# Performance work log

Measured on AMD Instinct MI355X. Metric: run time of the kernel, lower is better.

## Reference

```python
import jax, jax.numpy as jnp
import numpy as np

IMG = 128
NEAR, FAR = 1.0, 100.0
BG_EPS = 1e-3      # eps in soft_rasterize: background depth logit
SIGMA = 1e-6       # sigma_val
DIST_EPS = 1e-4    # dist_eps
GAMMA = 1e-6       # gamma_val
CHUNK = 500
B, V, F = 1, 5023, 10000


def setup_inputs():
    key = jax.random.key(0)
    k1, k2, k3, k4 = jax.random.split(key, 4)
    xy = jax.random.uniform(k1, (B, V, 2), minval=-1.0, maxval=1.0, dtype=jnp.float32)
    z = jax.random.uniform(k2, (B, V, 1), minval=5.0, maxval=15.0, dtype=jnp.float32)
    vertices = jnp.concatenate([xy, z], axis=-1)              # [B,V,3]
    faces = jax.random.randint(k3, (B, F, 3), 0, V, dtype=jnp.int32)
    attributes = jax.random.uniform(k4, (B, F, 3, 3), dtype=jnp.float32)
    return {"vertices": vertices, "faces": faces, "attributes": attributes}


def _seg_dist2(px, py, ax, ay, bx, by):
    # squared distance from pixel (px,py) to segment a-b; broadcasts [P] vs [B,C,1]
    dx = px - ax; dy = py - ay
    ex = bx - ax; ey = by - ay
    l2 = jnp.maximum(ex * ex + ey * ey, 1e-12)
    t = jnp.clip((dx * ex + dy * ey) / l2, 0.0, 1.0)
    rx = dx - t * ex; ry = dy - t * ey
    return rx * rx + ry * ry


def _render(vertices, faces, attributes):
    is_ = IMG
    P = is_ * is_
    bz = vertices.shape[0]
    v = vertices.at[..., 0].multiply(-1.0)                    # x flip (in-place in torch)
    fv = jax.vmap(lambda vv, ff: vv[ff])(v, faces)            # [B,F,3vert,3xyz]
    tex = attributes[..., :3]                                 # [B,F,3vert,3rgb]
    # fill_back=True: append copies with reversed winding
    fv = jnp.concatenate([fv, fv[:, :, ::-1, :]], axis=1)     # [B,2F,3,3]
    tex = jnp.concatenate([tex, tex[:, :, ::-1, :]], axis=1)
    F2 = fv.shape[1]
    pad = (-F2) % CHUNK
    valid = jnp.concatenate([jnp.ones((F2,), bool), jnp.zeros((pad,), bool)])
    fv = jnp.pad(fv, ((0, 0), (0, pad), (0, 0), (0, 0)))
    tex = jnp.pad(tex, ((0, 0), (0, pad), (0, 0), (0, 0)))
    n_chunks = (F2 + pad) // CHUNK
    fv = jnp.transpose(fv.reshape(bz, n_chunks, CHUNK, 3, 3), (1, 0, 2, 3, 4))
    tex = jnp.transpose(tex.reshape(bz, n_chunks, CHUNK, 3, 3), (1, 0, 2, 3, 4))
    valid = valid.reshape(n_chunks, CHUNK)

    # pixel centers in [-1,1]; row 0 is the top of the image (y flipped as in CUDA)
    xs = (2.0 * jnp.arange(is_, dtype=jnp.float32) + 1.0 - is_) / is_
    ys = (2.0 * (is_ - 1 - jnp.arange(is_, dtype=jnp.float32)) + 1.0 - is_) / is_
    px = jnp.broadcast_to(xs[None, :], (is_, is_)).reshape(-1)  # [P]
    py = jnp.broadcast_to(ys[:, None], (is_, is_)).reshape(-1)

    thr = DIST_EPS * SIGMA
    inv_g = 1.0 / GAMMA

    def step(carry, inp):
        m, s, cacc, prod = carry                # [B,P],[B,P],[B,3,P],[B,P]
        fvc, txc, vld = inp                     # [B,C,3,3],[B,C,3,3],[C]
        x0 = fvc[:, :, 0, 0][..., None]; y0 = fvc[:, :, 0, 1][..., None]; z0 = fvc[:, :, 0, 2][..., None]
        x1 = fvc[:, :, 1, 0][..., None]; y1 = fvc[:, :, 1, 1][..., None]; z1 = fvc[:, :, 1, 2][..., None]
        x2 = fvc[:, :, 2, 0][..., None]; y2 = fvc[:, :, 2, 1][..., None]; z2 = fvc[:, :, 2, 2][..., None]
        det = (y1 - y2) * (x0 - x2) + (x2 - x1) * (y0 - y2)   # [B,C,1]
        det = jnp.where(jnp.abs(det) < 1e-10, jnp.where(det < 0, -1e-10, 1e-10), det)
        w0 = ((y1 - y2) * (px - x2) + (x2 - x1) * (py - y2)) / det  # [B,C,P]
        w1 = ((y2 - y0) * (px - x2) + (x0 - x2) * (py - y2)) / det
        w2 = 1.0 - w0 - w1
        inside = (w0 >= 0) & (w1 >= 0) & (w2 >= 0)
        dis = jnp.minimum(jnp.minimum(_seg_dist2(px, py, x0, y0, x1, y1),
                                      _seg_dist2(px, py, x1, y1, x2, y2)),
                          _seg_dist2(px, py, x2, y2, x0, y0))     # [B,C,P] squared dist
        contrib = (inside | (dis < thr)) & vld[None, :, None]
        sgn = jnp.where(inside, 1.0, -1.0)
        Dp = jnp.where(contrib, jax.nn.sigmoid(sgn * dis / SIGMA), 0.0)
        prod = prod * jnp.prod(1.0 - Dp, axis=1)                  # alpha: prod(1-D)
        # clipped barycentric + perspective-correct depth
        c0 = jnp.clip(w0, 0.0, 1.0); c1 = jnp.clip(w1, 0.0, 1.0); c2 = jnp.clip(w2, 0.0, 1.0)
        csum = jnp.maximum(c0 + c1 + c2, 1e-5)
        c0 = c0 / csum; c1 = c1 / csum; c2 = c2 / csum
        zp_inv = c0 / z0 + c1 / z1 + c2 / z2
        zp = 1.0 / jnp.where(jnp.abs(zp_inv) < 1e-12, 1e-12, zp_inv)
        front = (y2 - y0) * (x1 - x0) < (y1 - y0) * (x2 - x0)     # [B,C,1]
        rgb_m = contrib & front & (zp >= NEAR) & (zp <= FAR)
        zpn = (FAR - zp) / (FAR - NEAR)
        new_m = jnp.maximum(m, jnp.max(jnp.where(rgb_m, zpn, -jnp.inf), axis=1))
        e = jnp.exp(jnp.where(rgb_m, (zpn - new_m[:, None, :]) * inv_g, -jnp.inf)) * Dp
        scale = jnp.exp((m - new_m) * inv_g)                      # [B,P]
        wc = jnp.stack([c0, c1, c2], axis=2)                      # [B,C,3,P]
        col = jnp.einsum('bcvp,bcvk->bckp', wc, txc)              # interpolated rgb
        s = s * scale + jnp.sum(e, axis=1)
        cacc = cacc * scale[:, None, :] + jnp.sum(e[:, :, None, :] * col, axis=1)
        return (new_m, s, cacc, prod), None

    m0 = jnp.full((bz, P), BG_EPS, jnp.float32)   # background logit = eps
    s0 = jnp.ones((bz, P), jnp.float32)           # exp((eps - m0)/gamma) = 1
    c0_ = jnp.zeros((bz, 3, P), jnp.float32)      # black background
    p0 = jnp.ones((bz, P), jnp.float32)
    (m, s, cacc, prod), _ = jax.lax.scan(jax.checkpoint(step), (m0, s0, c0_, p0), (fv, tex, valid))
    rgb = cacc / s[:, None, :]
    alpha = 1.0 - prod
    return jnp.concatenate([rgb, alpha[:, None, :]], axis=1).reshape(bz, 4, is_, is_)


def reference(vertices, faces, attributes):
    return _render(vertices, faces, attributes)
```

## Files before the change

kernel.cpp:

```cpp
#include <hip/hip_runtime.h>
#include <math.h>


#define NFACE 10000
#define IMG   128
#define P_TOT (IMG*IMG)
#define FSTR  40
#define NTILE 64
#define NQ    4
#define CAPQ  2500
#define CAP   (CAPQ*NQ)
#define BMAX  4096
#define NB    1024
#define CH    256
#define NCH   40
#define Z_LO  0.85f
#define Z_W   (0.12f/1024.0f)

__device__ __forceinline__ float rcp_nr(float x) {
    float r = __builtin_amdgcn_rcpf(x);
    r = r * __builtin_fmaf(-x, r, 2.0f);
    return r;
}

__device__ __forceinline__ float segd(float px, float py, float ax, float ay,
                                      float bx, float by, float il) {
    float dx = px - ax, dy = py - ay;
    float ex = bx - ax, ey = by - ay;
    float t = (dx * ex + dy * ey) * il;
    t = fminf(fmaxf(t, 0.0f), 1.0f);
    float rx = dx - t * ex, ry = dy - t * ey;
    return rx * rx + ry * ry;
}

__device__ __forceinline__ float rfl_f(float x) {
    return __uint_as_float(__builtin_amdgcn_readfirstlane(__float_as_uint(x)));
}

__device__ __forceinline__ int zbucket(float zub) {
    int b = (int)((zub - Z_LO) * (1.0f / Z_W));
    return min(max(b, 0), NB - 1);
}

__global__ __launch_bounds__(256) void k_prehist(const float* __restrict__ v,
                                                 const int* __restrict__ fc,
                                                 const float* __restrict__ at,
                                                 float* __restrict__ fb,
                                                 int* __restrict__ hist) {
    __shared__ int lh[NB];
    int c = blockIdx.x, tid = threadIdx.x;
    for (int j = tid; j < NB; j += 256) lh[j] = 0;
    __syncthreads();

    int f = c * CH + tid;
    if (f < NFACE) {
        int i0 = fc[3 * f], i1 = fc[3 * f + 1], i2 = fc[3 * f + 2];
        float x0 = -v[3 * i0], y0 = v[3 * i0 + 1], z0 = v[3 * i0 + 2];
        float x1 = -v[3 * i1], y1 = v[3 * i1 + 1], z1 = v[3 * i1 + 2];
        float x2 = -v[3 * i2], y2 = v[3 * i2 + 1], z2 = v[3 * i2 + 2];

        float det = (y1 - y2) * (x0 - x2) + (x2 - x1) * (y0 - y2);
        if (fabsf(det) < 1e-10f) det = (det < 0.0f) ? -1e-10f : 1e-10f;
        float a0 = y1 - y2, b0 = x2 - x1, a1 = y2 - y0, b1 = x0 - x2, detp = det;
        if (det < 0.0f) { detp = -det; a0 = -a0; b0 = -b0; a1 = -a1; b1 = -b1; }

        float a2 = a0 + a1, b2 = b0 + b1;
        float g0 = fmaxf(sqrtf(a0 * a0 + b0 * b0), 1e-12f);
        float g1 = fmaxf(sqrtf(a1 * a1 + b1 * b1), 1e-12f);
        float g2 = fmaxf(sqrtf(a2 * a2 + b2 * b2), 1e-12f);
        const float MARG = 3e-5f, AG = 1e-9f;
        float m0 = -(MARG * g0 + AG), m1 = -(MARG * g1 + AG), m2 = -(MARG * g2 + AG);

        float e01x = x1 - x0, e01y = y1 - y0;
        float e12x = x2 - x1, e12y = y2 - y1;
        float e20x = x0 - x2, e20y = y0 - y2;
        float il01 = 1.0f / fmaxf(e01x * e01x + e01y * e01y, 1e-12f);
        float il12 = 1.0f / fmaxf(e12x * e12x + e12y * e12y, 1e-12f);
        float il20 = 1.0f / fmaxf(e20x * e20x + e20y * e20y, 1e-12f);

        const float BM = 2e-5f;
        float bxmin = fminf(fminf(x0, x1), x2) - BM, bxmax = fmaxf(fmaxf(x0, x1), x2) + BM;
        float bymin = fminf(fminf(y0, y1), y2) - BM, bymax = fmaxf(fmaxf(y0, y1), y2) + BM;

        int mult = (((y2 - y0) * (x1 - x0)) < ((y1 - y0) * (x2 - x0)))
                 + (((y0 - y2) * (x1 - x2)) < ((y1 - y2) * (x0 - x2)));

        float zmin = fminf(fminf(z0, z1), z2);
        float zub = (100.0f - zmin) / 99.0f + 2e-6f;

        float* F = fb + (size_t)f * FSTR;
        F[0] = bxmin; F[1] = bxmax; F[2] = bymin; F[3] = bymax;
        F[4] = x2; F[5] = y2; F[6] = a0; F[7] = b0;
        F[8] = a1; F[9] = b1; F[10] = detp; F[11] = zub;
        F[12] = m0; F[13] = m1; F[14] = m2; F[15] = (float)mult;
        F[16] = x0; F[17] = y0; F[18] = x1; F[19] = y1;
        F[20] = il01; F[21] = il12; F[22] = il20; F[23] = 1.0f / detp;
        F[24] = 1.0f / z0; F[25] = 1.0f / z1; F[26] = 1.0f / z2;
        F[27] = 1.0f / g0; F[28] = 1.0f / g1; F[29] = 1.0f / g2;
#pragma unroll
        for (int k = 0; k < 9; k++) F[30 + k] = at[(size_t)f * 9 + k];
        F[39] = 0.0f;

        atomicAdd(&lh[zbucket(zub)], 1);
    }
    __syncthreads();
    for (int j = tid; j < NB; j += 256) hist[c * NB + j] = lh[j];
}

__global__ __launch_bounds__(1024) void k_scan(int* __restrict__ hist) {
    __shared__ int a[NB];
    int t = threadIdx.x;
    int tot = 0;
    for (int c = 0; c < NCH; c++) tot += hist[c * NB + t];
    a[t] = tot;
    for (int off = 1; off < NB; off <<= 1) {
        __syncthreads();
        int v = a[t] + ((t + off < NB) ? a[t + off] : 0);
        __syncthreads();
        a[t] = v;
    }
    int r = a[t] - tot;
    for (int c = 0; c < NCH; c++) {
        int h = hist[c * NB + t];
        hist[c * NB + t] = r;
        r += h;
    }
}

__global__ __launch_bounds__(256) void k_scatterre(const float* __restrict__ fb,
                                                   const int* __restrict__ hist,
                                                   float* __restrict__ fb2) {
    __shared__ int sb[CH];
    int c = blockIdx.x, tid = threadIdx.x;
    int f = c * CH + tid;
    bool valid = (f < NFACE);
    int b = valid ? zbucket(fb[(size_t)f * FSTR + 11]) : -1;
    sb[tid] = b;
    __syncthreads();
    if (valid) {
        int rank = 0;
        for (int j = 0; j < CH; j++) {
            int v2 = sb[j];
            rank += (j < tid && v2 == b) ? 1 : 0;
        }
        int pos = hist[c * NB + b] + rank;
        const float4* src = (const float4*)(fb + (size_t)f * FSTR);
        float4* dst = (float4*)(fb2 + (size_t)pos * FSTR);
#pragma unroll
        for (int k = 0; k < 10; k++) dst[k] = src[k];
        fb2[(size_t)pos * FSTR + 11] = Z_LO + (float)(b + 1) * Z_W + 1e-7f;
    }
}

__global__ __launch_bounds__(256) void k_bin(const float* __restrict__ fb2,
                                             float2* __restrict__ tmeta,
                                             int* __restrict__ cnt4) {
    int t = blockIdx.x >> 2, q = blockIdx.x & 3;
    int tid = threadIdx.x, wv = tid >> 6, lane = tid & 63;
    int tx = t & 7, ty = t >> 3;
    float x_lo = (float)(2 * (tx * 16) + 1 - IMG) / (float)IMG;
    float x_hi = (float)(2 * (tx * 16 + 15) + 1 - IMG) / (float)IMG;
    float y_hi = (float)(127 - 2 * (ty * 16)) / (float)IMG;
    float y_lo = (float)(127 - 2 * (ty * 16 + 15)) / (float)IMG;
    float cx = 0.5f * (x_lo + x_hi), hx = 0.5f * (x_hi - x_lo);
    float cy = 0.5f * (y_lo + y_hi), hy = 0.5f * (y_hi - y_lo);

    __shared__ int wc[4];
    int cnt = 0;
    int f0 = q * CAPQ;
    for (int base = f0; base < f0 + CAPQ; base += 256) {
        int j = base + tid;
        bool ov = false;
        float zub = 0.0f;
        if (j < f0 + CAPQ) {
            const float4* H = (const float4*)(fb2 + (size_t)j * FSTR);
            float4 h0 = H[0], h1 = H[1], h2 = H[2], h3 = H[3];
            ov = (h0.x <= x_hi) & (h0.y >= x_lo) & (h0.z <= y_hi) & (h0.w >= y_lo);
            if (ov) {
                float dx = cx - h1.x, dy = cy - h1.y;
                float mx0 = h1.z * dx + h1.w * dy + fabsf(h1.z) * hx + fabsf(h1.w) * hy;
                float mx1 = h2.x * dx + h2.y * dy + fabsf(h2.x) * hx + fabsf(h2.y) * hy;
                float A2 = -(h1.z + h2.x), B2 = -(h1.w + h2.y);
                float mx2 = h2.z + A2 * dx + B2 * dy + fabsf(A2) * hx + fabsf(B2) * hy;
                ov = (mx0 >= h3.x) & (mx1 >= h3.y) & (mx2 >= h3.z);
                zub = h2.w;
            }
        }
        unsigned long long mask = __ballot(ov);
        if (lane == 0) wc[wv] = __popcll(mask);
        __syncthreads();
        int off = cnt;
        for (int w = 0; w < 4; ++w) {
            if (w < wv) off += wc[w];
        }
        if (ov) {
            int pos = off + __popcll(mask & ((1ull << lane) - 1ull));
            tmeta[(size_t)t * CAP + q * CAPQ + pos] =
                make_float2(zub, __int_as_float(j));
        }
        cnt += wc[0] + wc[1] + wc[2] + wc[3];
        __syncthreads();
    }
    if (tid == 0) cnt4[t * 4 + q] = cnt;
}

__global__ __launch_bounds__(64) void k_map(const int* __restrict__ cnt4,
                                            int* __restrict__ map,
                                            int* __restrict__ starts,
                                            int* __restrict__ segs,
                                            int B) {
    int lane = threadIdx.x;
    int len = cnt4[4 * lane] + cnt4[4 * lane + 1] + cnt4[4 * lane + 2] + cnt4[4 * lane + 3];
    int tot = len;
    for (int o = 32; o > 0; o >>= 1) tot += __shfl_down(tot, o);
    tot = __shfl(tot, 0);
    int St = max(1, (int)(((long long)len * (long long)(B - NTILE)) /
                          (long long)max(tot, 1)));
    __shared__ int sS[64], sP[64];
    sS[lane] = St;
    __syncthreads();
    if (lane == 0) {
        int acc = 0;
        for (int t = 0; t < 64; ++t) { sP[t] = acc; acc += sS[t]; }
    }
    __syncthreads();
    for (int i = lane; i < B; i += 64) map[i] = -1;
    __syncthreads();
    int st = sP[lane];
    starts[lane] = st;
    segs[lane] = St;
    for (int s = 0; s < St; ++s) map[st + s] = (lane << 16) | s;
}

__global__ __launch_bounds__(256) void k_main(const float* __restrict__ fb2,
                                              const float2* __restrict__ tmeta,
                                              const int* __restrict__ cnt4,
                                              const int* __restrict__ map,
                                              const int* __restrict__ segs,
                                              float* __restrict__ part) {
    int bid = blockIdx.x;
    int mv = map[bid];
    if (mv < 0) return;
    int t = mv >> 16, seg = mv & 0xffff;
    int S = segs[t];

    int tid = threadIdx.x;
    int tx = t & 7, ty = t >> 3;
    int col = tx * 16 + (tid & 15);
    int row = ty * 16 + (tid >> 4);
    float px = (float)(2 * col + 1 - IMG) / (float)IMG;
    float py = (float)(2 * (IMG - 1 - row) + 1 - IMG) / (float)IMG;

    const float2* pm = tmeta + (size_t)t * CAP;

    float m = -__builtin_inff();
    float s = 0.0f, ca = 0.0f, cb = 0.0f, cc = 0.0f, pr = 1.0f;

    const float NEAR_T = 4.3e-3f;
    const float ZM = 1.3e-4f;

    bool done = false;
    for (int q = 0; q < 4 && !done; ++q) {
        int qlen = cnt4[t * 4 + q];
        for (int i = seg; i < qlen; i += S) {
            float2 mt = pm[q * CAPQ + i];
            float zcur = rfl_f(mt.x);
            if (__all((pr == 0.0f) & (zcur <= m - ZM))) { done = true; break; }
            int fj = __builtin_amdgcn_readfirstlane(__float_as_int(mt.y));
            const float4* H = (const float4*)(fb2 + (size_t)fj * FSTR);
            float4 g0 = H[0], g1 = H[1], g2 = H[2], g3 = H[3];

            bool inbox = (px >= g0.x) & (px <= g0.y) & (py >= g0.z) & (py <= g0.w);
            if (!__any(inbox)) continue;

            float x2 = g1.x, y2 = g1.y;
            float dx2 = px - x2, dy2 = py - y2;
            float num0 = g1.z * dx2 + g1.w * dy2;
            float num1 = g2.x * dx2 + g2.y * dy2;
            float detp = g2.z;
            float num2 = detp - num0 - num1;
            bool maybe = inbox & (num0 >= g3.x) & (num1 >= g3.y) & (num2 >= g3.z);
            if (!__any(maybe)) continue;

            const float* F = fb2 + (size_t)fj * FSTR;

            bool inside = (num0 >= 0.0f) & (num1 >= 0.0f) & (num2 >= 0.0f);
            bool inside_l = inside & inbox;

            float lin0 = num0 * F[27];
            float lin1 = num1 * F[28];
            float lin2 = num2 * F[29];
            float lbmin = fminf(fminf(lin0, lin1), lin2);

            bool outNear = maybe & (!inside);
            bool nearIn  = inside_l & (lbmin < NEAR_T);
            bool anyNear = __any(nearIn | outNear);

            float dis = 1e9f;
            float Dp;
            if (anyNear) {
                bool needAll = __any(outNear);
                float x0 = F[16], y0 = F[17], x1 = F[18], y1 = F[19];
                float d01 = 1e9f, d12 = 1e9f, d20 = 1e9f;
                if (needAll | __any(inside_l & (lin2 < NEAR_T)))
                    d01 = segd(px, py, x0, y0, x1, y1, F[20]);
                if (needAll | __any(inside_l & (lin0 < NEAR_T)))
                    d12 = segd(px, py, x1, y1, x2, y2, F[21]);
                if (needAll | __any(inside_l & (lin1 < NEAR_T)))
                    d20 = segd(px, py, x2, y2, x0, y0, F[22]);
                dis = fminf(fminf(d01, d12), d20);

                float qq = dis * 1e6f;
                float xs_ = inside ? qq : -qq;
                float tt = __expf(-fabsf(xs_));
                float Dpn = (xs_ >= 0.0f ? 1.0f : tt) * rcp_nr(1.0f + tt);
                bool nearl = nearIn | outNear;
                Dp = nearl ? Dpn : (inside_l ? 1.0f : 0.0f);
            } else {
                Dp = inside_l ? 1.0f : 0.0f;
            }

            bool contrib = inside_l | (outNear & (dis < 1e-10f));
            Dp = contrib ? Dp : 0.0f;
            float omd = 1.0f - Dp;
            pr *= contrib ? (omd * omd) : 1.0f;

            float multf = g3.w;
            bool doz = contrib & (multf > 0.0f);
            if (__any(doz & (zcur > m - ZM))) {
                float rdetp = F[23];
                float w0 = num0 * rdetp;
                float w1 = num1 * rdetp;
                float c0 = fminf(fmaxf(w0, 0.0f), 1.0f);
                float c1 = fminf(fmaxf(w1, 0.0f), 1.0f);
                float c2 = fminf(fmaxf(1.0f - w0 - w1, 0.0f), 1.0f);
                float csum = fmaxf(c0 + c1 + c2, 1e-5f);
                float rcs = rcp_nr(csum);
                c0 *= rcs; c1 *= rcs; c2 *= rcs;
                float zpi = c0 * F[24] + c1 * F[25] + c2 * F[26];
                if (fabsf(zpi) < 1e-12f) zpi = 1e-12f;
                float zp = rcp_nr(zpi);
                if (doz & (zp >= 1.0f) & (zp <= 100.0f)) {
                    float zpn = (100.0f - zp) / 99.0f;
                    if (zpn > m) {
                        float scl = __expf((m - zpn) * 1e6f);
                        s *= scl; ca *= scl; cb *= scl; cc *= scl;
                        m = zpn;
                    }
                    float arg = (zpn - m) * 1e6f;
                    if (arg > -110.0f) {
                        float e = __expf(arg) * Dp * multf;
                        float col0 = c0 * F[30] + c1 * F[33] + c2 * F[36];
                        float col1 = c0 * F[31] + c1 * F[34] + c2 * F[37];
                        float col2 = c0 * F[32] + c1 * F[35] + c2 * F[38];
                        s += e; ca += e * col0; cb += e * col1; cc += e * col2;
                    }
                }
            }
        }
    }

    size_t pb = (size_t)bid * 6 * 256;
    part[pb + 0 * 256 + tid] = m;
    part[pb + 1 * 256 + tid] = s;
    part[pb + 2 * 256 + tid] = ca;
    part[pb + 3 * 256 + tid] = cb;
    part[pb + 4 * 256 + tid] = cc;
    part[pb + 5 * 256 + tid] = pr;
}

__global__ __launch_bounds__(1024) void k_reduce(const float* __restrict__ part,
                                                 const int* __restrict__ starts,
                                                 const int* __restrict__ segs,
                                                 float* __restrict__ out) {
    __shared__ float sm[4][256], ss[4][256], sa[4][256], sb2[4][256],
                     sc[4][256], sp[4][256];
    int t = blockIdx.x;
    int tid = threadIdx.x;
    int q = tid & 255, sub = tid >> 8;
    int start = starts[t], S = segs[t];

    const float NINF = -__builtin_inff();
    float mp = NINF;
    for (int sgi = sub; sgi < S; sgi += 4)
        mp = fmaxf(mp, part[((size_t)(start + sgi) * 6 + 0) * 256 + q]);
    float sum = 0.0f, a = 0.0f, b = 0.0f, c = 0.0f, pr = 1.0f;
    for (int sgi = sub; sgi < S; sgi += 4) {
        const float* r = part + ((size_t)(start + sgi) * 6) * 256;
        float rm = r[0 * 256 + q];
        float w = (rm == NINF) ? 0.0f : __expf((rm - mp) * 1e6f);
        pr *= r[5 * 256 + q];
        if (__any(w != 0.0f)) {
            sum += r[1 * 256 + q] * w;
            a += r[2 * 256 + q] * w;
            b += r[3 * 256 + q] * w;
            c += r[4 * 256 + q] * w;
        }
    }
    sm[sub][q] = mp; ss[sub][q] = sum; sa[sub][q] = a;
    sb2[sub][q] = b; sc[sub][q] = c;  sp[sub][q] = pr;
    __syncthreads();
    if (sub == 0) {
        int tx = t & 7, ty = t >> 3;
        int col = tx * 16 + (q & 15);
        int row = ty * 16 + (q >> 4);
        int p = row * IMG + col;
        float M = 0.001f;
#pragma unroll
        for (int k = 0; k < 4; k++) M = fmaxf(M, sm[k][q]);
        float SUM = __expf((0.001f - M) * 1e6f);
        float A = 0.0f, B2 = 0.0f, C = 0.0f, PR = 1.0f;
#pragma unroll
        for (int k = 0; k < 4; k++) {
            float w = __expf((sm[k][q] - M) * 1e6f);
            SUM += ss[k][q] * w;
            A += sa[k][q] * w;
            B2 += sb2[k][q] * w;
            C += sc[k][q] * w;
            PR *= sp[k][q];
        }
        out[0 * P_TOT + p] = A / SUM;
        out[1 * P_TOT + p] = B2 / SUM;
        out[2 * P_TOT + p] = C / SUM;
        out[3 * P_TOT + p] = 1.0f - PR;
    }
}

extern "C" void kernel_launch(void* const* d_in, const int* in_sizes, int n_in,
                              void* d_out, int out_size, void* d_ws, size_t ws_size,
                              hipStream_t stream) {
    const float* verts = (const float*)d_in[0];
    const int*   faces = (const int*)d_in[1];
    const float* attrs = (const float*)d_in[2];
    float* out = (float*)d_out;
    float* ws  = (float*)d_ws;

    float*  fb    = ws;
    int*    hist  = (int*)(fb + (size_t)NFACE * FSTR);
    float*  fb2   = (float*)(hist + NCH * NB);
    float2* tmeta = (float2*)(fb2 + (size_t)NFACE * FSTR);
    int*    cnt4  = (int*)(tmeta + (size_t)NTILE * CAP);
    int*    map   = cnt4 + NTILE * 4;
    int*    starts= map + BMAX;
    int*    segs  = starts + NTILE;
    float*  part  = (float*)(segs + NTILE);

    size_t used_f = 2 * (size_t)NFACE * FSTR + NCH * NB
                  + 2 * (size_t)NTILE * CAP + NTILE * 4 + BMAX + 2 * NTILE;
    long   rem_f  = (long)(ws_size / 4) - (long)used_f;
    int B = (int)(rem_f / (6 * 256));
    if (B > BMAX) B = BMAX;
    if (B < 256)  B = 256;

    k_prehist<<<NCH, 256, 0, stream>>>(verts, faces, attrs, fb, hist);
    k_scan<<<1, 1024, 0, stream>>>(hist);
    k_scatterre<<<NCH, 256, 0, stream>>>(fb, hist, fb2);
    k_bin<<<NTILE * NQ, 256, 0, stream>>>(fb2, tmeta, cnt4);
    k_map<<<1, 64, 0, stream>>>(cnt4, map, starts, segs, B);
    k_main<<<B, 256, 0, stream>>>(fb2, tmeta, cnt4, map, segs, part);
    k_reduce<<<NTILE, 1024, 0, stream>>>(part, starts, segs, out);
}
```

Measured before the change: 139.1 us.

## Split each main-kernel block into four single-wavefront strip blocks

```diff
diff --git a/kernel.cpp b/kernel.cpp
--- a/kernel.cpp
+++ b/kernel.cpp
@@ -232,22 +232,22 @@
     for (int s = 0; s < St; ++s) map[st + s] = (lane << 16) | s;
 }
 
-__global__ __launch_bounds__(256) void k_main(const float* __restrict__ fb2,
-                                              const float2* __restrict__ tmeta,
-                                              const int* __restrict__ cnt4,
-                                              const int* __restrict__ map,
-                                              const int* __restrict__ segs,
-                                              float* __restrict__ part) {
-    int bid = blockIdx.x;
+__global__ __launch_bounds__(64) void k_main(const float* __restrict__ fb2,
+                                             const float2* __restrict__ tmeta,
+                                             const int* __restrict__ cnt4,
+                                             const int* __restrict__ map,
+                                             const int* __restrict__ segs,
+                                             float* __restrict__ part) {
+    int bid = blockIdx.x >> 2, strip = blockIdx.x & 3;
     int mv = map[bid];
     if (mv < 0) return;
     int t = mv >> 16, seg = mv & 0xffff;
     int S = segs[t];
 
-    int tid = threadIdx.x;
+    int lane = threadIdx.x;
     int tx = t & 7, ty = t >> 3;
-    int col = tx * 16 + (tid & 15);
-    int row = ty * 16 + (tid >> 4);
+    int col = tx * 16 + (lane & 15);
+    int row = ty * 16 + strip * 4 + (lane >> 4);
     float px = (float)(2 * col + 1 - IMG) / (float)IMG;
     float py = (float)(2 * (IMG - 1 - row) + 1 - IMG) / (float)IMG;
 
@@ -360,13 +360,13 @@
         }
     }
 
-    size_t pb = (size_t)bid * 6 * 256;
-    part[pb + 0 * 256 + tid] = m;
-    part[pb + 1 * 256 + tid] = s;
-    part[pb + 2 * 256 + tid] = ca;
-    part[pb + 3 * 256 + tid] = cb;
-    part[pb + 4 * 256 + tid] = cc;
-    part[pb + 5 * 256 + tid] = pr;
+    size_t pb = (size_t)blockIdx.x * 6 * 64;
+    part[pb + 0 * 64 + lane] = m;
+    part[pb + 1 * 64 + lane] = s;
+    part[pb + 2 * 64 + lane] = ca;
+    part[pb + 3 * 64 + lane] = cb;
+    part[pb + 4 * 64 + lane] = cc;
+    part[pb + 5 * 64 + lane] = pr;
 }
 
 __global__ __launch_bounds__(1024) void k_reduce(const float* __restrict__ part,
@@ -379,22 +379,23 @@
     int tid = threadIdx.x;
     int q = tid & 255, sub = tid >> 8;
     int start = starts[t], S = segs[t];
+    int strip = q >> 6, lane = q & 63;
 
     const float NINF = -__builtin_inff();
     float mp = NINF;
     for (int sgi = sub; sgi < S; sgi += 4)
-        mp = fmaxf(mp, part[((size_t)(start + sgi) * 6 + 0) * 256 + q]);
+        mp = fmaxf(mp, part[((size_t)((start + sgi) * 4 + strip) * 6 + 0) * 64 + lane]);
     float sum = 0.0f, a = 0.0f, b = 0.0f, c = 0.0f, pr = 1.0f;
     for (int sgi = sub; sgi < S; sgi += 4) {
-        const float* r = part + ((size_t)(start + sgi) * 6) * 256;
-        float rm = r[0 * 256 + q];
+        const float* r = part + ((size_t)((start + sgi) * 4 + strip) * 6) * 64;
+        float rm = r[0 * 64 + lane];
         float w = (rm == NINF) ? 0.0f : __expf((rm - mp) * 1e6f);
-        pr *= r[5 * 256 + q];
+        pr *= r[5 * 64 + lane];
         if (__any(w != 0.0f)) {
-            sum += r[1 * 256 + q] * w;
-            a += r[2 * 256 + q] * w;
-            b += r[3 * 256 + q] * w;
-            c += r[4 * 256 + q] * w;
+            sum += r[1 * 64 + lane] * w;
+            a += r[2 * 64 + lane] * w;
+            b += r[3 * 64 + lane] * w;
+            c += r[4 * 64 + lane] * w;
         }
     }
     sm[sub][q] = mp; ss[sub][q] = sum; sa[sub][q] = a;
@@ -402,8 +403,8 @@
     __syncthreads();
     if (sub == 0) {
         int tx = t & 7, ty = t >> 3;
-        int col = tx * 16 + (q & 15);
-        int row = ty * 16 + (q >> 4);
+        int col = tx * 16 + (lane & 15);
+        int row = ty * 16 + strip * 4 + (lane >> 4);
         int p = row * IMG + col;
         float M = 0.001f;
 #pragma unroll
@@ -457,6 +458,6 @@
     k_scatterre<<<NCH, 256, 0, stream>>>(fb, hist, fb2);
     k_bin<<<NTILE * NQ, 256, 0, stream>>>(fb2, tmeta, cnt4);
     k_map<<<1, 64, 0, stream>>>(cnt4, map, starts, segs, B);
-    k_main<<<B, 256, 0, stream>>>(fb2, tmeta, cnt4, map, segs, part);
+    k_main<<<B * 4, 64, 0, stream>>>(fb2, tmeta, cnt4, map, segs, part);
     k_reduce<<<NTILE, 1024, 0, stream>>>(part, starts, segs, out);
 }
```

Measured after the change: 150.5 us. +8.2%, slower.
